# Performance work log

Measured on AMD Instinct MI355X. Metric: run time of the kernel, lower is better.

The kernel has to match this reference:

```python
import jax, jax.numpy as jnp
import numpy as np

B, T, IN, H, OUT, SIM = 256, 128, 128, 1024, 256, 4
EPS_BN = 1e-5
EPS_COS = 1e-8
NEG_SLOPE = 0.2


def setup_inputs() -> dict:
    key = jax.random.key(0)
    ks = jax.random.split(key, 12)
    rn = lambda k, s: jax.random.normal(k, s, dtype=jnp.float32) * 0.05
    return {
        "x": jax.random.normal(ks[0], (B, T, IN), dtype=jnp.float32),
        "W_emb": rn(ks[1], (H, IN)),
        "b_emb": jnp.zeros((H,), jnp.float32),
        "gamma": jnp.ones((H,), jnp.float32),
        "beta": jnp.zeros((H,), jnp.float32),
        "memory": jax.random.normal(ks[2], (1, T, H), dtype=jnp.float32),
        "w_ih_x": rn(ks[3], (3 * OUT, H)),
        "w_hh_x": rn(ks[4], (3 * OUT, OUT)),
        "b_ih_x": jnp.zeros((3 * OUT,), jnp.float32),
        "b_hh_x": jnp.zeros((3 * OUT,), jnp.float32),
        "w_ih_m": rn(ks[5], (3 * OUT, H)),
        "w_hh_m": rn(ks[6], (3 * OUT, OUT)),
        "b_ih_m": jnp.zeros((3 * OUT,), jnp.float32),
        "b_hh_m": jnp.zeros((3 * OUT,), jnp.float32),
        "W_sx": rn(ks[7], (SIM, OUT)),
        "b_sx": jnp.zeros((SIM,), jnp.float32),
        "W_sm": rn(ks[8], (SIM, OUT)),
        "b_sm": jnp.zeros((SIM,), jnp.float32),
    }


def _gru(x, h, w_ih, w_hh, b_ih, b_hh):
    # PyTorch GRUCell math
    gi = x @ w_ih.T + b_ih
    gh = h @ w_hh.T + b_hh
    i_r, i_z, i_n = jnp.split(gi, 3, axis=-1)
    h_r, h_z, h_n = jnp.split(gh, 3, axis=-1)
    r = jax.nn.sigmoid(i_r + h_r)
    z = jax.nn.sigmoid(i_z + h_z)
    n = jnp.tanh(i_n + r * h_n)
    return (1.0 - z) * n + z * h


def _forward(x, W_emb, b_emb, gamma, beta, memory,
             w_ih_x, w_hh_x, b_ih_x, b_hh_x,
             w_ih_m, w_hh_m, b_ih_m, b_hh_m,
             W_sx, b_sx, W_sm, b_sm):
    # embed + LeakyReLU(0.2)
    e = x @ W_emb.T + b_emb                                  # (B,T,H)
    e = jnp.where(e >= 0, e, NEG_SLOPE * e)
    # BatchNorm1d, training mode: per-channel stats over (B,T), biased var
    mean = jnp.mean(e, axis=(0, 1))
    var = jnp.mean((e - mean) ** 2, axis=(0, 1))
    e = (e - mean) * jax.lax.rsqrt(var + EPS_BN) * gamma + beta

    mem = memory[0]                                          # (T,H) shared across batch
    b = x.shape[0]

    def step(carry, inps):
        hx, hm = carry
        xt, mt = inps                                        # (B,H), (H,)
        mtb = jnp.broadcast_to(mt, (b, mt.shape[-1]))
        hx = _gru(xt, hx, w_ih_x, w_hh_x, b_ih_x, b_hh_x)    # (B,OUT)
        hm = _gru(mtb, hm, w_ih_m, w_hh_m, b_ih_m, b_hh_m)   # (B,OUT)
        # cosine-similarity addressing between sim_size projections
        qx = hx @ W_sx.T + b_sx                              # (B,SIM)
        qm = hm @ W_sm.T + b_sm
        num = jnp.sum(qx * qm, axis=-1)
        den = (jnp.maximum(jnp.linalg.norm(qx, axis=-1), EPS_COS)
               * jnp.maximum(jnp.linalg.norm(qm, axis=-1), EPS_COS))
        g = jax.nn.sigmoid(num / den)[:, None]               # gate in (0,1)
        out = g * hx + (1.0 - g) * hm
        return (hx, hm), out

    h0 = (jnp.zeros((b, OUT), e.dtype), jnp.zeros((b, OUT), e.dtype))
    (_, _), outs = jax.lax.scan(step, h0, (e.transpose(1, 0, 2), mem))
    return outs[-1].reshape(-1, OUT)                         # out of last timestep


def reference(x, W_emb, b_emb, gamma, beta, memory,
              w_ih_x, w_hh_x, b_ih_x, b_hh_x,
              w_ih_m, w_hh_m, b_ih_m, b_hh_m,
              W_sx, b_sx, W_sm, b_sm):
    return _forward(x, W_emb, b_emb, gamma, beta, memory,
                    w_ih_x, w_hh_x, b_ih_x, b_hh_x,
                    w_ih_m, w_hh_m, b_ih_m, b_hh_m,
                    W_sx, b_sx, W_sm, b_sm)
```

## Files before the change

kernel.cpp:

```cpp
#include <hip/hip_runtime.h>
#include <stdint.h>


typedef float  f32x4 __attribute__((ext_vector_type(4)));
typedef __bf16 bf16x8 __attribute__((ext_vector_type(8)));

#define B_   256
#define T_   128
#define IN_  128
#define H_   1024
#define OUT_ 256
#define M_   32768

static constexpr size_t OFF_XB    = 0;
static constexpr size_t OFF_WEMB  = 8388608;
static constexpr size_t OFF_WHX   = 8650752;
static constexpr size_t OFF_WHM   = 9043968;
static constexpr size_t OFF_SUM   = 9437184;
static constexpr size_t OFF_SSQ   = 9441280;
static constexpr size_t OFF_SCALE = 9445376;
static constexpr size_t OFF_CC    = 9449472;
static constexpr size_t OFF_BIASX = 9453568;
static constexpr size_t OFF_GIM   = 9457664;
static constexpr size_t OFF_EACT  = 9654272;
static constexpr size_t OFF_GI    = 76763136;
static constexpr size_t OFF_HXF   = 127094784;
static constexpr size_t OFF_HMF   = 127356928;
static constexpr size_t OFF_WPX   = 127373312;

__device__ __forceinline__ float sigmoidf_(float x) {
    return __builtin_amdgcn_rcpf(1.0f + __expf(-x));
}
__device__ __forceinline__ float tanhf_(float x) {
    return 1.0f - 2.0f * __builtin_amdgcn_rcpf(1.0f + __expf(2.0f * x));
}
__device__ __forceinline__ void gload_lds16(const void* g, void* l) {
    __builtin_amdgcn_global_load_lds(
        (const __attribute__((address_space(1))) unsigned int*)g,
        (__attribute__((address_space(3))) unsigned int*)l, 16, 0, 0);
}

__global__ void prep(const float* __restrict__ x, const float* __restrict__ wemb,
                     const float* __restrict__ whx, const float* __restrict__ whm,
                     __bf16* __restrict__ xb, __bf16* __restrict__ wembb,
                     __bf16* __restrict__ whxb, __bf16* __restrict__ whmb,
                     float* __restrict__ stats )
{
    long i = (long)blockIdx.x * 256 + threadIdx.x;
    if (i < 2048) stats[i] = 0.0f;
    if (i < 4194304)      xb[i] = (__bf16)x[i];
    else if (i < 4325376) wembb[i - 4194304] = (__bf16)wemb[i - 4194304];
    else if (i < 4521984) whxb[i - 4325376]  = (__bf16)whx[i - 4325376];
    else if (i < 4718592) whmb[i - 4521984]  = (__bf16)whm[i - 4521984];
}

template<int MODE>
__launch_bounds__(256)
__global__ void gemm_nt(const __bf16* __restrict__ A, const __bf16* __restrict__ Bm,
                        const float* __restrict__ bias, __bf16* __restrict__ C,
                        float* __restrict__ sums, float* __restrict__ ssqs,
                        int K, int N)
{
    __shared__ __bf16 As[128 * 32];
    __shared__ __bf16 Bs[128 * 32];
    const int tid  = threadIdx.x;
    const int lane = tid & 63;
    const int wv   = tid >> 6;
    const int wm   = wv >> 1, wn = wv & 1;
    const int l15  = lane & 15, quad = lane >> 4;
    const long m0 = (long)blockIdx.x * 128;
    const long n0 = (long)blockIdx.y * 128;

    const int srow = lane >> 2;
    const int scol = (lane & 3) * 8;
    const __bf16* ag[2]; const __bf16* bg[2];
    __bf16* al[2]; __bf16* bl[2];
#pragma unroll
    for (int j = 0; j < 2; j++) {
        const int s = wv * 2 + j;
        ag[j] = A  + (m0 + s * 16 + srow) * K + scol;
        bg[j] = Bm + (n0 + s * 16 + srow) * K + scol;
        al[j] = &As[s * 512];
        bl[j] = &Bs[s * 512];
    }

    const f32x4 fz = {0.f, 0.f, 0.f, 0.f};
    f32x4 acc[4][4];
#pragma unroll
    for (int i = 0; i < 4; i++)
#pragma unroll
        for (int j = 0; j < 4; j++) acc[i][j] = fz;

    for (int k0 = 0; k0 < K; k0 += 32) {
        __syncthreads();
        gload_lds16(ag[0] + k0, al[0]);
        gload_lds16(ag[1] + k0, al[1]);
        gload_lds16(bg[0] + k0, bl[0]);
        gload_lds16(bg[1] + k0, bl[1]);
        __syncthreads();
        bf16x8 af[4], bfr[4];
#pragma unroll
        for (int mt = 0; mt < 4; mt++)
            af[mt] = *(const bf16x8*)(&As[(wm * 64 + mt * 16 + l15) * 32 + quad * 8]);
#pragma unroll
        for (int nt = 0; nt < 4; nt++)
            bfr[nt] = *(const bf16x8*)(&Bs[(wn * 64 + nt * 16 + l15) * 32 + quad * 8]);
#pragma unroll
        for (int mt = 0; mt < 4; mt++)
#pragma unroll
            for (int nt = 0; nt < 4; nt++)
                acc[mt][nt] = __builtin_amdgcn_mfma_f32_16x16x32_bf16(af[mt], bfr[nt], acc[mt][nt], 0, 0, 0);
    }

#pragma unroll
    for (int nt = 0; nt < 4; nt++) {
        const long ncol = n0 + wn * 64 + nt * 16 + l15;
        const float bi = bias[ncol];
        float s = 0.f, ss = 0.f;
#pragma unroll
        for (int mt = 0; mt < 4; mt++) {
#pragma unroll
            for (int r = 0; r < 4; r++) {
                float v = acc[mt][nt][r] + bi;
                if (MODE == 0) v = (v >= 0.f) ? v : 0.2f * v;
                __bf16 hv = (__bf16)v;
                C[(m0 + wm * 64 + mt * 16 + quad * 4 + r) * (long)N + ncol] = hv;
                if (MODE == 0) { float fv = (float)hv; s += fv; ss += fv * fv; }
            }
        }
        if (MODE == 0) {
            s += __shfl_xor(s, 16);  ss += __shfl_xor(ss, 16);
            s += __shfl_xor(s, 32);  ss += __shfl_xor(ss, 32);
            if (lane < 16) {
                atomicAdd(&sums[n0 + wn * 64 + nt * 16 + lane], s);
                atomicAdd(&ssqs[n0 + wn * 64 + nt * 16 + lane], ss);
            }
        }
    }
}

__global__ void finalize_stats(const float* __restrict__ sums, const float* __restrict__ ssqs,
                               const float* __restrict__ gamma, const float* __restrict__ beta,
                               float* __restrict__ scale, float* __restrict__ cc)
{
    int h = threadIdx.x;
    const float inv = 1.0f / 32768.0f;
    float mean = sums[h] * inv;
    float var  = ssqs[h] * inv - mean * mean;
    float s    = rsqrtf(var + 1e-5f) * gamma[h];
    scale[h] = s;
    cc[h]    = beta[h] - mean * s;
}

__global__ void build_wp(const float* __restrict__ w_ih_x, const float* __restrict__ b_ih_x,
                         const float* __restrict__ b_hh_x, const float* __restrict__ scale,
                         const float* __restrict__ cc, __bf16* __restrict__ wpx,
                         float* __restrict__ biasx)
{
    const int j = blockIdx.x;
    const int lane = threadIdx.x;
    float accv = 0.f;
#pragma unroll
    for (int i = 0; i < 16; i++) {
        int h = i * 64 + lane;
        float w = w_ih_x[(long)j * 1024 + h];
        wpx[(long)j * 1024 + h] = (__bf16)(w * scale[h]);
        accv += cc[h] * w;
    }
    for (int off = 32; off; off >>= 1) accv += __shfl_xor(accv, off);
    if (lane == 0) biasx[j] = accv + b_ih_x[j] + (j < 512 ? b_hh_x[j] : 0.0f);
}

__global__ void build_gim(const float* __restrict__ memory, const float* __restrict__ w_ih_m,
                          const float* __restrict__ b_ih_m, const float* __restrict__ b_hh_m,
                          __bf16* __restrict__ gim)
{
    const int j = blockIdx.x;
    const int t0 = blockIdx.y * 32;
    const int lane = threadIdx.x;
    float w[16];
#pragma unroll
    for (int i = 0; i < 16; i++) w[i] = w_ih_m[(long)j * 1024 + i * 64 + lane];
    const float bb = b_ih_m[j] + (j < 512 ? b_hh_m[j] : 0.0f);
    for (int t = t0; t < t0 + 32; t++) {
        float s = 0.f;
#pragma unroll
        for (int i = 0; i < 16; i++) s += w[i] * memory[(long)t * 1024 + i * 64 + lane];
        for (int off = 32; off; off >>= 1) s += __shfl_xor(s, off);
        if (lane == 0) gim[t * 768 + j] = (__bf16)(s + bb);
    }
}

__launch_bounds__(512, 2)
__global__ void recurrence(const __bf16* __restrict__ gi, const __bf16* __restrict__ gim,
                           const __bf16* __restrict__ whx, const __bf16* __restrict__ whm,
                           const float* __restrict__ bhhx, const float* __restrict__ bhhm,
                           float* __restrict__ hxfin, float* __restrict__ hmfin)
{
    __shared__ __bf16 hxl[2][16 * 264];
    __shared__ __bf16 gil[2][16 * 776];
    const int wg   = blockIdx.x;
    const int tid  = threadIdx.x;
    const int lane = tid & 63;
    const int v    = tid >> 6;
    const int l15  = lane & 15, quad = lane >> 4;
    const bool isX = (wg < 16);
    const __bf16* wh    = isX ? whx : whm;
    const float*  bhh   = isX ? bhhx : bhhm;
    const __bf16* gbase = isX ? gi : gim;

    bf16x8 W[6][8];
#pragma unroll
    for (int nt = 0; nt < 6; nt++) {
        const int g = nt >> 1, ct = nt & 1;
        const long j = g * 256 + (v * 2 + ct) * 16 + l15;
#pragma unroll
        for (int kt = 0; kt < 8; kt++)
            W[nt][kt] = *(const bf16x8*)(wh + j * 256 + kt * 32 + quad * 8);
    }
    float bhhn[2];
#pragma unroll
    for (int ct = 0; ct < 2; ct++) bhhn[ct] = bhh[512 + v * 32 + ct * 16 + l15];

    for (int i = tid; i < 16 * 264; i += 512) hxl[0][i] = (__bf16)0.f;

    float st[8];
#pragma unroll
    for (int i = 0; i < 8; i++) st[i] = 0.f;

    const int r0 = v * 2, r1 = r0 + 1;
    const long grow0 = isX ? (long)((wg * 16 + r0) * 128) * 768 : 0;
    const long grow1 = isX ? (long)((wg * 16 + r1) * 128) * 768 : 0;

    {
        const __bf16* p0 = gbase + grow0;
        const __bf16* p1 = gbase + grow1;
        gload_lds16(p0 + (long)lane * 8, &gil[0][r0 * 776]);
        gload_lds16(p1 + (long)lane * 8, &gil[0][r1 * 776]);
        if (lane < 32) {
            gload_lds16(p0 + 512 + (long)lane * 8, &gil[0][r0 * 776 + 512]);
            gload_lds16(p1 + 512 + (long)lane * 8, &gil[0][r1 * 776 + 512]);
        }
    }
    __syncthreads();

    int cur = 0;
    for (int t = 0; t < 128; t++) {
        if (t < 127) {
            const __bf16* p0 = gbase + grow0 + (long)(t + 1) * 768;
            const __bf16* p1 = gbase + grow1 + (long)(t + 1) * 768;
            __bf16* dst = &gil[(t + 1) & 1][0];
            gload_lds16(p0 + (long)lane * 8, dst + r0 * 776);
            gload_lds16(p1 + (long)lane * 8, dst + r1 * 776);
            if (lane < 32) {
                gload_lds16(p0 + 512 + (long)lane * 8, dst + r0 * 776 + 512);
                gload_lds16(p1 + 512 + (long)lane * 8, dst + r1 * 776 + 512);
            }
        }

        const f32x4 fz = {0.f, 0.f, 0.f, 0.f};
        f32x4 acc[6];
#pragma unroll
        for (int nt = 0; nt < 6; nt++) acc[nt] = fz;
        const __bf16* hxc = &hxl[cur][0];
#pragma unroll
        for (int kt = 0; kt < 8; kt++) {
            bf16x8 a = *(const bf16x8*)(hxc + l15 * 264 + kt * 32 + quad * 8);
#pragma unroll
            for (int nt = 0; nt < 6; nt++)
                acc[nt] = __builtin_amdgcn_mfma_f32_16x16x32_bf16(a, W[nt][kt], acc[nt], 0, 0, 0);
        }

        const int nxt = cur ^ 1;
        __bf16* hxn = &hxl[nxt][0];
        const __bf16* gcur = &gil[t & 1][0];
#pragma unroll
        for (int ct = 0; ct < 2; ct++) {
            const int ob = v * 32 + ct * 16 + l15;
#pragma unroll
            for (int r = 0; r < 4; r++) {
                const int row = quad * 4 + r;
                const float gr = (float)gcur[row * 776 + ob];
                const float gz = (float)gcur[row * 776 + 256 + ob];
                const float gn = (float)gcur[row * 776 + 512 + ob];
                const float rg = sigmoidf_(gr + acc[ct][r]);
                const float zg = sigmoidf_(gz + acc[2 + ct][r]);
                const float ng = tanhf_(gn + rg * (acc[4 + ct][r] + bhhn[ct]));
                float h = st[ct * 4 + r];
                h = ng + zg * (h - ng);
                st[ct * 4 + r] = h;
                hxn[row * 264 + ob] = (__bf16)h;
            }
        }
        __syncthreads();
        cur = nxt;
    }

    float* finp = isX ? (hxfin + (long)wg * 16 * 256) : hmfin;
#pragma unroll
    for (int ct = 0; ct < 2; ct++) {
        const int ob = v * 32 + ct * 16 + l15;
#pragma unroll
        for (int r = 0; r < 4; r++)
            finp[(quad * 4 + r) * 256 + ob] = st[ct * 4 + r];
    }
}

__global__ void finalize(const float* __restrict__ hxfin, const float* __restrict__ hmfin,
                         const float* __restrict__ W_sx, const float* __restrict__ b_sx,
                         const float* __restrict__ W_sm, const float* __restrict__ b_sm,
                         float* __restrict__ out)
{
    const int b = blockIdx.x;
    const int lane = threadIdx.x;
    float qx[4], qm[4];
#pragma unroll
    for (int s = 0; s < 4; s++) {
        float px = 0.f, pm = 0.f;
#pragma unroll
        for (int i = 0; i < 4; i++) {
            int h = i * 64 + lane;
            px += W_sx[s * 256 + h] * hxfin[b * 256 + h];
            pm += W_sm[s * 256 + h] * hmfin[h];
        }
        for (int off = 32; off; off >>= 1) { px += __shfl_xor(px, off); pm += __shfl_xor(pm, off); }
        qx[s] = px + b_sx[s];
        qm[s] = pm + b_sm[s];
    }
    float num = 0.f, nx = 0.f, nm = 0.f;
#pragma unroll
    for (int s = 0; s < 4; s++) { num += qx[s] * qm[s]; nx += qx[s] * qx[s]; nm += qm[s] * qm[s]; }
    const float den = fmaxf(sqrtf(nx), 1e-8f) * fmaxf(sqrtf(nm), 1e-8f);
    const float g = 1.0f / (1.0f + __expf(-num / den));
#pragma unroll
    for (int i = 0; i < 4; i++) {
        int h = i * 64 + lane;
        out[b * 256 + h] = g * hxfin[b * 256 + h] + (1.0f - g) * hmfin[h];
    }
}

extern "C" void kernel_launch(void* const* d_in, const int* in_sizes, int n_in,
                              void* d_out, int out_size, void* d_ws, size_t ws_size,
                              hipStream_t stream)
{
    (void)in_sizes; (void)n_in; (void)out_size; (void)ws_size;
    const float* x      = (const float*)d_in[0];
    const float* W_emb  = (const float*)d_in[1];
    const float* b_emb  = (const float*)d_in[2];
    const float* gamma  = (const float*)d_in[3];
    const float* beta   = (const float*)d_in[4];
    const float* memory = (const float*)d_in[5];
    const float* w_ih_x = (const float*)d_in[6];
    const float* w_hh_x = (const float*)d_in[7];
    const float* b_ih_x = (const float*)d_in[8];
    const float* b_hh_x = (const float*)d_in[9];
    const float* w_ih_m = (const float*)d_in[10];
    const float* w_hh_m = (const float*)d_in[11];
    const float* b_ih_m = (const float*)d_in[12];
    const float* b_hh_m = (const float*)d_in[13];
    const float* W_sx   = (const float*)d_in[14];
    const float* b_sx   = (const float*)d_in[15];
    const float* W_sm   = (const float*)d_in[16];
    const float* b_sm   = (const float*)d_in[17];
    float* out = (float*)d_out;
    char* ws = (char*)d_ws;

    __bf16* xb    = (__bf16*)(ws + OFF_XB);
    __bf16* wembb = (__bf16*)(ws + OFF_WEMB);
    __bf16* whxb  = (__bf16*)(ws + OFF_WHX);
    __bf16* whmb  = (__bf16*)(ws + OFF_WHM);
    float*  sums  = (float*)(ws + OFF_SUM);
    float*  ssqs  = (float*)(ws + OFF_SSQ);
    float*  scale = (float*)(ws + OFF_SCALE);
    float*  cc    = (float*)(ws + OFF_CC);
    float*  biasx = (float*)(ws + OFF_BIASX);
    __bf16* gim   = (__bf16*)(ws + OFF_GIM);
    __bf16* eact  = (__bf16*)(ws + OFF_EACT);
    __bf16* gi    = (__bf16*)(ws + OFF_GI);
    float*  hxf   = (float*)(ws + OFF_HXF);
    float*  hmf   = (float*)(ws + OFF_HMF);
    __bf16* wpx   = (__bf16*)(ws + OFF_WPX);

    prep<<<18432, 256, 0, stream>>>(x, W_emb, w_hh_x, w_hh_m, xb, wembb, whxb, whmb, sums);
    gemm_nt<0><<<dim3(256, 8), 256, 0, stream>>>(xb, wembb, b_emb, eact, sums, ssqs, 128, 1024);
    finalize_stats<<<1, 1024, 0, stream>>>(sums, ssqs, gamma, beta, scale, cc);
    build_wp<<<768, 64, 0, stream>>>(w_ih_x, b_ih_x, b_hh_x, scale, cc, wpx, biasx);
    build_gim<<<dim3(768, 4), 64, 0, stream>>>(memory, w_ih_m, b_ih_m, b_hh_m, gim);
    gemm_nt<1><<<dim3(256, 6), 256, 0, stream>>>(eact, wpx, biasx, gi, sums, ssqs, 1024, 768);
    recurrence<<<17, 512, 0, stream>>>(gi, gim, whxb, whmb, b_hh_x, b_hh_m, hxf, hmf);
    finalize<<<256, 64, 0, stream>>>(hxf, hmf, W_sx, b_sx, W_sm, b_sm, out);
}
```

Measured before the change: 492.4 us.

## Split recurrence over 16 waves per block and fold BN stats into build_wp

The recurrence kernel now runs 1024 threads (16 waves) per block, each wave owning 16 output columns and one batch row's gate prefetch, instead of 8 waves each owning 32 columns. This halves the per-wave MFMA chain and register-held weights on the sequential critical path, and doubles latency hiding per step. The cost is heavier __syncthreads across more waves. Separately, the finalize_stats launch is removed, and each build_wp block recomputes mean and scale inline, trading redundant work for one fewer kernel launch.

```diff
diff --git a/kernel.cpp b/kernel.cpp
--- a/kernel.cpp
+++ b/kernel.cpp
@@ -139,33 +139,26 @@
     }
 }
 
-__global__ void finalize_stats(const float* __restrict__ sums, const float* __restrict__ ssqs,
-                               const float* __restrict__ gamma, const float* __restrict__ beta,
-                               float* __restrict__ scale, float* __restrict__ cc)
-{
-    int h = threadIdx.x;
-    const float inv = 1.0f / 32768.0f;
-    float mean = sums[h] * inv;
-    float var  = ssqs[h] * inv - mean * mean;
-    float s    = rsqrtf(var + 1e-5f) * gamma[h];
-    scale[h] = s;
-    cc[h]    = beta[h] - mean * s;
-}
-
 __global__ void build_wp(const float* __restrict__ w_ih_x, const float* __restrict__ b_ih_x,
-                         const float* __restrict__ b_hh_x, const float* __restrict__ scale,
-                         const float* __restrict__ cc, __bf16* __restrict__ wpx,
+                         const float* __restrict__ b_hh_x, const float* __restrict__ sums,
+                         const float* __restrict__ ssqs, const float* __restrict__ gamma,
+                         const float* __restrict__ beta, __bf16* __restrict__ wpx,
                          float* __restrict__ biasx)
 {
     const int j = blockIdx.x;
     const int lane = threadIdx.x;
+    const float inv = 1.0f / 32768.0f;
     float accv = 0.f;
 #pragma unroll
     for (int i = 0; i < 16; i++) {
         int h = i * 64 + lane;
+        float mean = sums[h] * inv;
+        float var  = ssqs[h] * inv - mean * mean;
+        float s    = rsqrtf(var + 1e-5f) * gamma[h];
+        float c    = beta[h] - mean * s;
         float w = w_ih_x[(long)j * 1024 + h];
-        wpx[(long)j * 1024 + h] = (__bf16)(w * scale[h]);
-        accv += cc[h] * w;
+        wpx[(long)j * 1024 + h] = (__bf16)(w * s);
+        accv += c * w;
     }
     for (int off = 32; off; off >>= 1) accv += __shfl_xor(accv, off);
     if (lane == 0) biasx[j] = accv + b_ih_x[j] + (j < 512 ? b_hh_x[j] : 0.0f);
@@ -191,7 +184,7 @@
     }
 }
 
-__launch_bounds__(512, 2)
+__launch_bounds__(1024, 4)
 __global__ void recurrence(const __bf16* __restrict__ gi, const __bf16* __restrict__ gim,
                            const __bf16* __restrict__ whx, const __bf16* __restrict__ whm,
                            const float* __restrict__ bhhx, const float* __restrict__ bhhm,
@@ -209,88 +202,72 @@
     const float*  bhh   = isX ? bhhx : bhhm;
     const __bf16* gbase = isX ? gi : gim;
 
-    bf16x8 W[6][8];
-#pragma unroll
-    for (int nt = 0; nt < 6; nt++) {
-        const int g = nt >> 1, ct = nt & 1;
-        const long j = g * 256 + (v * 2 + ct) * 16 + l15;
+    bf16x8 W[3][8];
+#pragma unroll
+    for (int g = 0; g < 3; g++) {
+        const long j = g * 256 + v * 16 + l15;
 #pragma unroll
         for (int kt = 0; kt < 8; kt++)
-            W[nt][kt] = *(const bf16x8*)(wh + j * 256 + kt * 32 + quad * 8);
-    }
-    float bhhn[2];
-#pragma unroll
-    for (int ct = 0; ct < 2; ct++) bhhn[ct] = bhh[512 + v * 32 + ct * 16 + l15];
-
-    for (int i = tid; i < 16 * 264; i += 512) hxl[0][i] = (__bf16)0.f;
-
-    float st[8];
-#pragma unroll
-    for (int i = 0; i < 8; i++) st[i] = 0.f;
-
-    const int r0 = v * 2, r1 = r0 + 1;
-    const long grow0 = isX ? (long)((wg * 16 + r0) * 128) * 768 : 0;
-    const long grow1 = isX ? (long)((wg * 16 + r1) * 128) * 768 : 0;
+            W[g][kt] = *(const bf16x8*)(wh + j * 256 + kt * 32 + quad * 8);
+    }
+    const int ob = v * 16 + l15;
+    const float bhhn = bhh[512 + ob];
+
+    for (int i = tid; i < 16 * 264; i += 1024) hxl[0][i] = (__bf16)0.f;
+
+    float st[4];
+#pragma unroll
+    for (int i = 0; i < 4; i++) st[i] = 0.f;
+
+    const long grow = isX ? (long)((wg * 16 + v) * 128) * 768 : 0;
 
     {
-        const __bf16* p0 = gbase + grow0;
-        const __bf16* p1 = gbase + grow1;
-        gload_lds16(p0 + (long)lane * 8, &gil[0][r0 * 776]);
-        gload_lds16(p1 + (long)lane * 8, &gil[0][r1 * 776]);
-        if (lane < 32) {
-            gload_lds16(p0 + 512 + (long)lane * 8, &gil[0][r0 * 776 + 512]);
-            gload_lds16(p1 + 512 + (long)lane * 8, &gil[0][r1 * 776 + 512]);
-        }
+        const __bf16* p = gbase + grow;
+        gload_lds16(p + (long)lane * 8, &gil[0][v * 776]);
+        if (lane < 32)
+            gload_lds16(p + 512 + (long)lane * 8, &gil[0][v * 776 + 512]);
     }
     __syncthreads();
 
     int cur = 0;
     for (int t = 0; t < 128; t++) {
         if (t < 127) {
-            const __bf16* p0 = gbase + grow0 + (long)(t + 1) * 768;
-            const __bf16* p1 = gbase + grow1 + (long)(t + 1) * 768;
-            __bf16* dst = &gil[(t + 1) & 1][0];
-            gload_lds16(p0 + (long)lane * 8, dst + r0 * 776);
-            gload_lds16(p1 + (long)lane * 8, dst + r1 * 776);
-            if (lane < 32) {
-                gload_lds16(p0 + 512 + (long)lane * 8, dst + r0 * 776 + 512);
-                gload_lds16(p1 + 512 + (long)lane * 8, dst + r1 * 776 + 512);
-            }
+            const __bf16* p = gbase + grow + (long)(t + 1) * 768;
+            __bf16* dst = &gil[(t + 1) & 1][v * 776];
+            gload_lds16(p + (long)lane * 8, dst);
+            if (lane < 32)
+                gload_lds16(p + 512 + (long)lane * 8, dst + 512);
         }
 
         const f32x4 fz = {0.f, 0.f, 0.f, 0.f};
-        f32x4 acc[6];
-#pragma unroll
-        for (int nt = 0; nt < 6; nt++) acc[nt] = fz;
+        f32x4 acc[3];
+#pragma unroll
+        for (int g = 0; g < 3; g++) acc[g] = fz;
         const __bf16* hxc = &hxl[cur][0];
 #pragma unroll
         for (int kt = 0; kt < 8; kt++) {
             bf16x8 a = *(const bf16x8*)(hxc + l15 * 264 + kt * 32 + quad * 8);
 #pragma unroll
-            for (int nt = 0; nt < 6; nt++)
-                acc[nt] = __builtin_amdgcn_mfma_f32_16x16x32_bf16(a, W[nt][kt], acc[nt], 0, 0, 0);
+            for (int g = 0; g < 3; g++)
+                acc[g] = __builtin_amdgcn_mfma_f32_16x16x32_bf16(a, W[g][kt], acc[g], 0, 0, 0);
         }
 
         const int nxt = cur ^ 1;
         __bf16* hxn = &hxl[nxt][0];
         const __bf16* gcur = &gil[t & 1][0];
 #pragma unroll
-        for (int ct = 0; ct < 2; ct++) {
-            const int ob = v * 32 + ct * 16 + l15;
-#pragma unroll
-            for (int r = 0; r < 4; r++) {
-                const int row = quad * 4 + r;
-                const float gr = (float)gcur[row * 776 + ob];
-                const float gz = (float)gcur[row * 776 + 256 + ob];
-                const float gn = (float)gcur[row * 776 + 512 + ob];
-                const float rg = sigmoidf_(gr + acc[ct][r]);
-                const float zg = sigmoidf_(gz + acc[2 + ct][r]);
-                const float ng = tanhf_(gn + rg * (acc[4 + ct][r] + bhhn[ct]));
-                float h = st[ct * 4 + r];
-                h = ng + zg * (h - ng);
-                st[ct * 4 + r] = h;
-                hxn[row * 264 + ob] = (__bf16)h;
-            }
+        for (int r = 0; r < 4; r++) {
+            const int row = quad * 4 + r;
+            const float gr = (float)gcur[row * 776 + ob];
+            const float gz = (float)gcur[row * 776 + 256 + ob];
+            const float gn = (float)gcur[row * 776 + 512 + ob];
+            const float rg = sigmoidf_(gr + acc[0][r]);
+            const float zg = sigmoidf_(gz + acc[1][r]);
+            const float ng = tanhf_(gn + rg * (acc[2][r] + bhhn));
+            float h = st[r];
+            h = ng + zg * (h - ng);
+            st[r] = h;
+            hxn[row * 264 + ob] = (__bf16)h;
         }
         __syncthreads();
         cur = nxt;
@@ -298,12 +275,8 @@
 
     float* finp = isX ? (hxfin + (long)wg * 16 * 256) : hmfin;
 #pragma unroll
-    for (int ct = 0; ct < 2; ct++) {
-        const int ob = v * 32 + ct * 16 + l15;
-#pragma unroll
-        for (int r = 0; r < 4; r++)
-            finp[(quad * 4 + r) * 256 + ob] = st[ct * 4 + r];
-    }
+    for (int r = 0; r < 4; r++)
+        finp[(quad * 4 + r) * 256 + ob] = st[r];
 }
 
 __global__ void finalize(const float* __restrict__ hxfin, const float* __restrict__ hmfin,
@@ -371,8 +344,6 @@
     __bf16* whmb  = (__bf16*)(ws + OFF_WHM);
     float*  sums  = (float*)(ws + OFF_SUM);
     float*  ssqs  = (float*)(ws + OFF_SSQ);
-    float*  scale = (float*)(ws + OFF_SCALE);
-    float*  cc    = (float*)(ws + OFF_CC);
     float*  biasx = (float*)(ws + OFF_BIASX);
     __bf16* gim   = (__bf16*)(ws + OFF_GIM);
     __bf16* eact  = (__bf16*)(ws + OFF_EACT);
@@ -383,10 +354,9 @@
 
     prep<<<18432, 256, 0, stream>>>(x, W_emb, w_hh_x, w_hh_m, xb, wembb, whxb, whmb, sums);
     gemm_nt<0><<<dim3(256, 8), 256, 0, stream>>>(xb, wembb, b_emb, eact, sums, ssqs, 128, 1024);
-    finalize_stats<<<1, 1024, 0, stream>>>(sums, ssqs, gamma, beta, scale, cc);
-    build_wp<<<768, 64, 0, stream>>>(w_ih_x, b_ih_x, b_hh_x, scale, cc, wpx, biasx);
+    build_wp<<<768, 64, 0, stream>>>(w_ih_x, b_ih_x, b_hh_x, sums, ssqs, gamma, beta, wpx, biasx);
     build_gim<<<dim3(768, 4), 64, 0, stream>>>(memory, w_ih_m, b_ih_m, b_hh_m, gim);
     gemm_nt<1><<<dim3(256, 6), 256, 0, stream>>>(eact, wpx, biasx, gi, sums, ssqs, 1024, 768);
-    recurrence<<<17, 512, 0, stream>>>(gi, gim, whxb, whmb, b_hh_x, b_hh_m, hxf, hmf);
+    recurrence<<<17, 1024, 0, stream>>>(gi, gim, whxb, whmb, b_hh_x, b_hh_m, hxf, hmf);
     finalize<<<256, 64, 0, stream>>>(hxf, hmf, W_sx, b_sx, W_sm, b_sm, out);
 }
```

Measured after the change: 538.7 us. 9.4% more time.

## Overlap input-projection GEMM with recurrence via flag-synchronized fused kernel

Applied to the files above, without the earlier changes.

Merges the gi GEMM and the recurrence into one launch. Blocks 17 and up compute 128-row tiles of gi in time-major order and publish per-tile completion flags. The 17 recurrence blocks spin on those flags, so the sequential recurrence can start while later timesteps are still being projected. The BN stats finalization is folded into the weight-prep kernel, which now also builds gim, cutting several launches. The cost is spin-waiting, GEMM tiles shrinking to 128x128 with no double buffering, and reliance on the recurrence blocks being scheduled first and on forward progress.

```diff
diff --git a/kernel.cpp b/kernel.cpp
--- a/kernel.cpp
+++ b/kernel.cpp
@@ -18,8 +18,7 @@
 static constexpr size_t OFF_WHM   = 9043968;
 static constexpr size_t OFF_SUM   = 9437184;
 static constexpr size_t OFF_SSQ   = 9441280;
-static constexpr size_t OFF_SCALE = 9445376;
-static constexpr size_t OFF_CC    = 9449472;
+static constexpr size_t OFF_FLAGS = 9445376;
 static constexpr size_t OFF_BIASX = 9453568;
 static constexpr size_t OFF_GIM   = 9457664;
 static constexpr size_t OFF_EACT  = 9654272;
@@ -44,22 +43,22 @@
                      const float* __restrict__ whx, const float* __restrict__ whm,
                      __bf16* __restrict__ xb, __bf16* __restrict__ wembb,
                      __bf16* __restrict__ whxb, __bf16* __restrict__ whmb,
-                     float* __restrict__ stats )
+                     float* __restrict__ stats , int* __restrict__ flags )
 {
     long i = (long)blockIdx.x * 256 + threadIdx.x;
     if (i < 2048) stats[i] = 0.0f;
+    else if (i < 2304) flags[i - 2048] = 0;
     if (i < 4194304)      xb[i] = (__bf16)x[i];
     else if (i < 4325376) wembb[i - 4194304] = (__bf16)wemb[i - 4194304];
     else if (i < 4521984) whxb[i - 4325376]  = (__bf16)whx[i - 4325376];
     else if (i < 4718592) whmb[i - 4521984]  = (__bf16)whm[i - 4521984];
 }
 
-template<int MODE>
 __launch_bounds__(256)
-__global__ void gemm_nt(const __bf16* __restrict__ A, const __bf16* __restrict__ Bm,
-                        const float* __restrict__ bias, __bf16* __restrict__ C,
-                        float* __restrict__ sums, float* __restrict__ ssqs,
-                        int K, int N)
+__global__ void gemm_e(const __bf16* __restrict__ A, const __bf16* __restrict__ Bm,
+                       const float* __restrict__ bias, __bf16* __restrict__ C,
+                       float* __restrict__ sums, float* __restrict__ ssqs,
+                       int K, int N)
 {
     __shared__ __bf16 As[128 * 32];
     __shared__ __bf16 Bs[128 * 32];
@@ -122,88 +121,147 @@
 #pragma unroll
             for (int r = 0; r < 4; r++) {
                 float v = acc[mt][nt][r] + bi;
-                if (MODE == 0) v = (v >= 0.f) ? v : 0.2f * v;
+                v = (v >= 0.f) ? v : 0.2f * v;
                 __bf16 hv = (__bf16)v;
                 C[(m0 + wm * 64 + mt * 16 + quad * 4 + r) * (long)N + ncol] = hv;
-                if (MODE == 0) { float fv = (float)hv; s += fv; ss += fv * fv; }
+                float fv = (float)hv; s += fv; ss += fv * fv;
             }
         }
-        if (MODE == 0) {
-            s += __shfl_xor(s, 16);  ss += __shfl_xor(ss, 16);
-            s += __shfl_xor(s, 32);  ss += __shfl_xor(ss, 32);
-            if (lane < 16) {
-                atomicAdd(&sums[n0 + wn * 64 + nt * 16 + lane], s);
-                atomicAdd(&ssqs[n0 + wn * 64 + nt * 16 + lane], ss);
-            }
-        }
-    }
-}
-
-__global__ void finalize_stats(const float* __restrict__ sums, const float* __restrict__ ssqs,
-                               const float* __restrict__ gamma, const float* __restrict__ beta,
-                               float* __restrict__ scale, float* __restrict__ cc)
-{
-    int h = threadIdx.x;
-    const float inv = 1.0f / 32768.0f;
-    float mean = sums[h] * inv;
-    float var  = ssqs[h] * inv - mean * mean;
-    float s    = rsqrtf(var + 1e-5f) * gamma[h];
-    scale[h] = s;
-    cc[h]    = beta[h] - mean * s;
-}
-
-__global__ void build_wp(const float* __restrict__ w_ih_x, const float* __restrict__ b_ih_x,
-                         const float* __restrict__ b_hh_x, const float* __restrict__ scale,
-                         const float* __restrict__ cc, __bf16* __restrict__ wpx,
-                         float* __restrict__ biasx)
-{
-    const int j = blockIdx.x;
+        s += __shfl_xor(s, 16);  ss += __shfl_xor(ss, 16);
+        s += __shfl_xor(s, 32);  ss += __shfl_xor(ss, 32);
+        if (lane < 16) {
+            atomicAdd(&sums[n0 + wn * 64 + nt * 16 + lane], s);
+            atomicAdd(&ssqs[n0 + wn * 64 + nt * 16 + lane], ss);
+        }
+    }
+}
+
+__global__ void build_misc(const float* __restrict__ w_ih_x, const float* __restrict__ b_ih_x,
+                           const float* __restrict__ b_hh_x, const float* __restrict__ sums,
+                           const float* __restrict__ ssqs, const float* __restrict__ gamma,
+                           const float* __restrict__ beta, __bf16* __restrict__ wpx,
+                           float* __restrict__ biasx,
+                           const float* __restrict__ memory, const float* __restrict__ w_ih_m,
+                           const float* __restrict__ b_ih_m, const float* __restrict__ b_hh_m,
+                           __bf16* __restrict__ gim)
+{
     const int lane = threadIdx.x;
-    float accv = 0.f;
-#pragma unroll
-    for (int i = 0; i < 16; i++) {
-        int h = i * 64 + lane;
-        float w = w_ih_x[(long)j * 1024 + h];
-        wpx[(long)j * 1024 + h] = (__bf16)(w * scale[h]);
-        accv += cc[h] * w;
-    }
-    for (int off = 32; off; off >>= 1) accv += __shfl_xor(accv, off);
-    if (lane == 0) biasx[j] = accv + b_ih_x[j] + (j < 512 ? b_hh_x[j] : 0.0f);
-}
-
-__global__ void build_gim(const float* __restrict__ memory, const float* __restrict__ w_ih_m,
-                          const float* __restrict__ b_ih_m, const float* __restrict__ b_hh_m,
-                          __bf16* __restrict__ gim)
-{
-    const int j = blockIdx.x;
-    const int t0 = blockIdx.y * 32;
-    const int lane = threadIdx.x;
-    float w[16];
-#pragma unroll
-    for (int i = 0; i < 16; i++) w[i] = w_ih_m[(long)j * 1024 + i * 64 + lane];
-    const float bb = b_ih_m[j] + (j < 512 ? b_hh_m[j] : 0.0f);
-    for (int t = t0; t < t0 + 32; t++) {
-        float s = 0.f;
-#pragma unroll
-        for (int i = 0; i < 16; i++) s += w[i] * memory[(long)t * 1024 + i * 64 + lane];
-        for (int off = 32; off; off >>= 1) s += __shfl_xor(s, off);
-        if (lane == 0) gim[t * 768 + j] = (__bf16)(s + bb);
+    if (blockIdx.x < 768) {
+        const int j = blockIdx.x;
+        const float inv = 1.0f / 32768.0f;
+        float accv = 0.f;
+#pragma unroll
+        for (int i = 0; i < 16; i++) {
+            int h = i * 64 + lane;
+            float mean = sums[h] * inv;
+            float var  = ssqs[h] * inv - mean * mean;
+            float s    = rsqrtf(var + 1e-5f) * gamma[h];
+            float c    = beta[h] - mean * s;
+            float w = w_ih_x[(long)j * 1024 + h];
+            wpx[(long)j * 1024 + h] = (__bf16)(w * s);
+            accv += c * w;
+        }
+        for (int off = 32; off; off >>= 1) accv += __shfl_xor(accv, off);
+        if (lane == 0) biasx[j] = accv + b_ih_x[j] + (j < 512 ? b_hh_x[j] : 0.0f);
+    } else {
+        const int g = blockIdx.x - 768;
+        const int j = g & 1023 % 1024;
+        const int jj = g % 768;
+        const int t0 = (g / 768) * 32;
+        float w[16];
+#pragma unroll
+        for (int i = 0; i < 16; i++) w[i] = w_ih_m[(long)jj * 1024 + i * 64 + lane];
+        const float bb = b_ih_m[jj] + (jj < 512 ? b_hh_m[jj] : 0.0f);
+        for (int t = t0; t < t0 + 32; t++) {
+            float s = 0.f;
+#pragma unroll
+            for (int i = 0; i < 16; i++) s += w[i] * memory[(long)t * 1024 + i * 64 + lane];
+            for (int off = 32; off; off >>= 1) s += __shfl_xor(s, off);
+            if (lane == 0) gim[t * 768 + jj] = (__bf16)(s + bb);
+        }
+        (void)j;
     }
 }
 
 __launch_bounds__(512, 2)
-__global__ void recurrence(const __bf16* __restrict__ gi, const __bf16* __restrict__ gim,
-                           const __bf16* __restrict__ whx, const __bf16* __restrict__ whm,
-                           const float* __restrict__ bhhx, const float* __restrict__ bhhm,
-                           float* __restrict__ hxfin, float* __restrict__ hmfin)
-{
-    __shared__ __bf16 hxl[2][16 * 264];
-    __shared__ __bf16 gil[2][16 * 776];
-    const int wg   = blockIdx.x;
+__global__ void fused(const __bf16* __restrict__ eact, const __bf16* __restrict__ wpx,
+                      const float* __restrict__ biasx, __bf16* __restrict__ gi,
+                      const __bf16* __restrict__ gim,
+                      const __bf16* __restrict__ whx, const __bf16* __restrict__ whm,
+                      const float* __restrict__ bhhx, const float* __restrict__ bhhm,
+                      float* __restrict__ hxfin, float* __restrict__ hmfin,
+                      int* __restrict__ flags)
+{
+    __shared__ union {
+        struct { __bf16 hxl[2][16 * 264]; __bf16 gil[2][16 * 776]; } rec;
+        struct { __bf16 As[128 * 32]; __bf16 Bs[128 * 32]; } gm;
+        char pad[83968];
+    } sm;
+
     const int tid  = threadIdx.x;
     const int lane = tid & 63;
     const int v    = tid >> 6;
     const int l15  = lane & 15, quad = lane >> 4;
+
+    if (blockIdx.x >= 17) {
+        const int g  = blockIdx.x - 17;
+        const int mt = g / 6;
+        const long m0 = (long)mt * 128;
+        const long n0 = (long)(g % 6) * 128;
+        const int wm = v >> 1, wn = v & 1;
+
+        const int srow = lane >> 2;
+        const int scol = (lane & 3) * 8;
+        const long m = m0 + v * 16 + srow;
+        const __bf16* agA = eact + (((m & 255) << 7) + (m >> 8)) * 1024 + scol;
+        const __bf16* agB = wpx + (n0 + v * 16 + srow) * 1024 + scol;
+        __bf16* alA = &sm.gm.As[v * 512];
+        __bf16* alB = &sm.gm.Bs[v * 512];
+
+        const f32x4 fz = {0.f, 0.f, 0.f, 0.f};
+        f32x4 acc[2][4];
+#pragma unroll
+        for (int i = 0; i < 2; i++)
+#pragma unroll
+            for (int j = 0; j < 4; j++) acc[i][j] = fz;
+
+        for (int k0 = 0; k0 < 1024; k0 += 32) {
+            __syncthreads();
+            gload_lds16(agA + k0, alA);
+            gload_lds16(agB + k0, alB);
+            __syncthreads();
+            bf16x8 af[2], bfr[4];
+#pragma unroll
+            for (int i = 0; i < 2; i++)
+                af[i] = *(const bf16x8*)(&sm.gm.As[(wm * 32 + i * 16 + l15) * 32 + quad * 8]);
+#pragma unroll
+            for (int j = 0; j < 4; j++)
+                bfr[j] = *(const bf16x8*)(&sm.gm.Bs[(wn * 64 + j * 16 + l15) * 32 + quad * 8]);
+#pragma unroll
+            for (int i = 0; i < 2; i++)
+#pragma unroll
+                for (int j = 0; j < 4; j++)
+                    acc[i][j] = __builtin_amdgcn_mfma_f32_16x16x32_bf16(af[i], bfr[j], acc[i][j], 0, 0, 0);
+        }
+
+#pragma unroll
+        for (int j = 0; j < 4; j++) {
+            const long ncol = n0 + wn * 64 + j * 16 + l15;
+            const float bi = biasx[ncol];
+#pragma unroll
+            for (int i = 0; i < 2; i++)
+#pragma unroll
+                for (int r = 0; r < 4; r++)
+                    gi[(m0 + wm * 32 + i * 16 + quad * 4 + r) * 768 + ncol] =
+                        (__bf16)(acc[i][j][r] + bi);
+        }
+        __syncthreads();
+        if (tid == 0)
+            __hip_atomic_fetch_add(&flags[mt], 1, __ATOMIC_RELEASE, __HIP_MEMORY_SCOPE_AGENT);
+        return;
+    }
+
+    const int wg   = blockIdx.x;
     const bool isX = (wg < 16);
     const __bf16* wh    = isX ? whx : whm;
     const float*  bhh   = isX ? bhhx : bhhm;
@@ -212,8 +270,8 @@
     bf16x8 W[6][8];
 #pragma unroll
     for (int nt = 0; nt < 6; nt++) {
-        const int g = nt >> 1, ct = nt & 1;
-        const long j = g * 256 + (v * 2 + ct) * 16 + l15;
+        const int gg = nt >> 1, ct = nt & 1;
+        const long j = gg * 256 + (v * 2 + ct) * 16 + l15;
 #pragma unroll
         for (int kt = 0; kt < 8; kt++)
             W[nt][kt] = *(const bf16x8*)(wh + j * 256 + kt * 32 + quad * 8);
@@ -222,24 +280,36 @@
 #pragma unroll
     for (int ct = 0; ct < 2; ct++) bhhn[ct] = bhh[512 + v * 32 + ct * 16 + l15];
 
-    for (int i = tid; i < 16 * 264; i += 512) hxl[0][i] = (__bf16)0.f;
+    for (int i = tid; i < 16 * 264; i += 512) sm.rec.hxl[0][i] = (__bf16)0.f;
 
     float st[8];
 #pragma unroll
     for (int i = 0; i < 8; i++) st[i] = 0.f;
 
     const int r0 = v * 2, r1 = r0 + 1;
-    const long grow0 = isX ? (long)((wg * 16 + r0) * 128) * 768 : 0;
-    const long grow1 = isX ? (long)((wg * 16 + r1) * 128) * 768 : 0;
-
+    const long base0 = isX ? (long)(wg * 16 + r0) * 768 : 0;
+    const long base1 = isX ? (long)(wg * 16 + r1) * 768 : 0;
+    const long tstr  = isX ? (long)256 * 768 : 768;
+    const int  myhalf = wg >> 3;
+
+    int ready = -1;
+    if (isX) {
+        const int need = myhalf;
+        if (__hip_atomic_load(&flags[need], __ATOMIC_ACQUIRE, __HIP_MEMORY_SCOPE_AGENT) == 6) ready = need;
+        else {
+            while (__hip_atomic_load(&flags[need], __ATOMIC_ACQUIRE, __HIP_MEMORY_SCOPE_AGENT) != 6)
+                __builtin_amdgcn_s_sleep(2);
+            ready = need;
+        }
+    }
     {
-        const __bf16* p0 = gbase + grow0;
-        const __bf16* p1 = gbase + grow1;
-        gload_lds16(p0 + (long)lane * 8, &gil[0][r0 * 776]);
-        gload_lds16(p1 + (long)lane * 8, &gil[0][r1 * 776]);
+        const __bf16* p0 = gbase + base0;
+        const __bf16* p1 = gbase + base1;
+        gload_lds16(p0 + (long)lane * 8, &sm.rec.gil[0][r0 * 776]);
+        gload_lds16(p1 + (long)lane * 8, &sm.rec.gil[0][r1 * 776]);
         if (lane < 32) {
-            gload_lds16(p0 + 512 + (long)lane * 8, &gil[0][r0 * 776 + 512]);
-            gload_lds16(p1 + 512 + (long)lane * 8, &gil[0][r1 * 776 + 512]);
+            gload_lds16(p0 + 512 + (long)lane * 8, &sm.rec.gil[0][r0 * 776 + 512]);
+            gload_lds16(p1 + 512 + (long)lane * 8, &sm.rec.gil[0][r1 * 776 + 512]);
         }
     }
     __syncthreads();
@@ -247,9 +317,22 @@
     int cur = 0;
     for (int t = 0; t < 128; t++) {
         if (t < 127) {
-            const __bf16* p0 = gbase + grow0 + (long)(t + 1) * 768;
-            const __bf16* p1 = gbase + grow1 + (long)(t + 1) * 768;
-            __bf16* dst = &gil[(t + 1) & 1][0];
+            if (isX) {
+                const int need = 2 * (t + 1) + myhalf;
+                if (need > ready) {
+                    int probe = need + 14; if (probe > 255) probe = 255;
+                    if (__hip_atomic_load(&flags[probe], __ATOMIC_ACQUIRE, __HIP_MEMORY_SCOPE_AGENT) == 6)
+                        ready = probe;
+                    else {
+                        while (__hip_atomic_load(&flags[need], __ATOMIC_ACQUIRE, __HIP_MEMORY_SCOPE_AGENT) != 6)
+                            __builtin_amdgcn_s_sleep(2);
+                        ready = need;
+                    }
+                }
+            }
+            const __bf16* p0 = gbase + base0 + (long)(t + 1) * tstr;
+            const __bf16* p1 = gbase + base1 + (long)(t + 1) * tstr;
+            __bf16* dst = &sm.rec.gil[(t + 1) & 1][0];
             gload_lds16(p0 + (long)lane * 8, dst + r0 * 776);
             gload_lds16(p1 + (long)lane * 8, dst + r1 * 776);
             if (lane < 32) {
@@ -262,7 +345,7 @@
         f32x4 acc[6];
 #pragma unroll
         for (int nt = 0; nt < 6; nt++) acc[nt] = fz;
-        const __bf16* hxc = &hxl[cur][0];
+        const __bf16* hxc = &sm.rec.hxl[cur][0];
 #pragma unroll
         for (int kt = 0; kt < 8; kt++) {
             bf16x8 a = *(const bf16x8*)(hxc + l15 * 264 + kt * 32 + quad * 8);
@@ -272,8 +355,8 @@
         }
 
         const int nxt = cur ^ 1;
-        __bf16* hxn = &hxl[nxt][0];
-        const __bf16* gcur = &gil[t & 1][0];
+        __bf16* hxn = &sm.rec.hxl[nxt][0];
+        const __bf16* gcur = &sm.rec.gil[t & 1][0];
 #pragma unroll
         for (int ct = 0; ct < 2; ct++) {
             const int ob = v * 32 + ct * 16 + l15;
@@ -371,8 +454,7 @@
     __bf16* whmb  = (__bf16*)(ws + OFF_WHM);
     float*  sums  = (float*)(ws + OFF_SUM);
     float*  ssqs  = (float*)(ws + OFF_SSQ);
-    float*  scale = (float*)(ws + OFF_SCALE);
-    float*  cc    = (float*)(ws + OFF_CC);
+    int*    flags = (int*)(ws + OFF_FLAGS);
     float*  biasx = (float*)(ws + OFF_BIASX);
     __bf16* gim   = (__bf16*)(ws + OFF_GIM);
     __bf16* eact  = (__bf16*)(ws + OFF_EACT);
@@ -381,12 +463,11 @@
     float*  hmf   = (float*)(ws + OFF_HMF);
     __bf16* wpx   = (__bf16*)(ws + OFF_WPX);
 
-    prep<<<18432, 256, 0, stream>>>(x, W_emb, w_hh_x, w_hh_m, xb, wembb, whxb, whmb, sums);
-    gemm_nt<0><<<dim3(256, 8), 256, 0, stream>>>(xb, wembb, b_emb, eact, sums, ssqs, 128, 1024);
-    finalize_stats<<<1, 1024, 0, stream>>>(sums, ssqs, gamma, beta, scale, cc);
-    build_wp<<<768, 64, 0, stream>>>(w_ih_x, b_ih_x, b_hh_x, scale, cc, wpx, biasx);
-    build_gim<<<dim3(768, 4), 64, 0, stream>>>(memory, w_ih_m, b_ih_m, b_hh_m, gim);
-    gemm_nt<1><<<dim3(256, 6), 256, 0, stream>>>(eact, wpx, biasx, gi, sums, ssqs, 1024, 768);
-    recurrence<<<17, 512, 0, stream>>>(gi, gim, whxb, whmb, b_hh_x, b_hh_m, hxf, hmf);
+    prep<<<18432, 256, 0, stream>>>(x, W_emb, w_hh_x, w_hh_m, xb, wembb, whxb, whmb, sums, flags);
+    gemm_e<<<dim3(256, 8), 256, 0, stream>>>(xb, wembb, b_emb, eact, sums, ssqs, 128, 1024);
+    build_misc<<<3840, 64, 0, stream>>>(w_ih_x, b_ih_x, b_hh_x, sums, ssqs, gamma, beta, wpx, biasx,
+                                        memory, w_ih_m, b_ih_m, b_hh_m, gim);
+    fused<<<17 + 1536, 512, 0, stream>>>(eact, wpx, biasx, gi, gim, whxb, whmb,
+                                         b_hh_x, b_hh_m, hxf, hmf, flags);
     finalize<<<256, 64, 0, stream>>>(hxf, hmf, W_sx, b_sx, W_sm, b_sm, out);
 }
```

Measured after the change: 490.2 us. About the same (-0.4%).

## Merge stats/weight-prep kernels and retile input-gate GEMM to 256x384 blocks

Applied to the files above, without the earlier changes.

Folds finalize_stats, build_wp and build_gim into one build_misc launch, recomputing the BN scale and shift inline per channel so the scale/cc buffers go away. The gi GEMM (K=1024, N=768) now uses a dedicated 1024-thread kernel with 256x384 tiles instead of the generic 128x128 template. Bigger tiles raise operand reuse and cut global reloads of A and B, and fewer launches cut launch overhead. The cost is 256 blocks, roughly one per CU, with more accumulators per thread, which may lower latency hiding. The k-loop is still unpipelined.

```diff
diff --git a/kernel.cpp b/kernel.cpp
--- a/kernel.cpp
+++ b/kernel.cpp
@@ -4,13 +4,6 @@
 
 typedef float  f32x4 __attribute__((ext_vector_type(4)));
 typedef __bf16 bf16x8 __attribute__((ext_vector_type(8)));
-
-#define B_   256
-#define T_   128
-#define IN_  128
-#define H_   1024
-#define OUT_ 256
-#define M_   32768
 
 static constexpr size_t OFF_XB    = 0;
 static constexpr size_t OFF_WEMB  = 8388608;
@@ -18,8 +11,6 @@
 static constexpr size_t OFF_WHM   = 9043968;
 static constexpr size_t OFF_SUM   = 9437184;
 static constexpr size_t OFF_SSQ   = 9441280;
-static constexpr size_t OFF_SCALE = 9445376;
-static constexpr size_t OFF_CC    = 9449472;
 static constexpr size_t OFF_BIASX = 9453568;
 static constexpr size_t OFF_GIM   = 9457664;
 static constexpr size_t OFF_EACT  = 9654272;
@@ -54,12 +45,11 @@
     else if (i < 4718592) whmb[i - 4521984]  = (__bf16)whm[i - 4521984];
 }
 
-template<int MODE>
 __launch_bounds__(256)
-__global__ void gemm_nt(const __bf16* __restrict__ A, const __bf16* __restrict__ Bm,
-                        const float* __restrict__ bias, __bf16* __restrict__ C,
-                        float* __restrict__ sums, float* __restrict__ ssqs,
-                        int K, int N)
+__global__ void gemm_e(const __bf16* __restrict__ A, const __bf16* __restrict__ Bm,
+                       const float* __restrict__ bias, __bf16* __restrict__ C,
+                       float* __restrict__ sums, float* __restrict__ ssqs,
+                       int K, int N)
 {
     __shared__ __bf16 As[128 * 32];
     __shared__ __bf16 Bs[128 * 32];
@@ -122,72 +112,126 @@
 #pragma unroll
             for (int r = 0; r < 4; r++) {
                 float v = acc[mt][nt][r] + bi;
-                if (MODE == 0) v = (v >= 0.f) ? v : 0.2f * v;
+                v = (v >= 0.f) ? v : 0.2f * v;
                 __bf16 hv = (__bf16)v;
                 C[(m0 + wm * 64 + mt * 16 + quad * 4 + r) * (long)N + ncol] = hv;
-                if (MODE == 0) { float fv = (float)hv; s += fv; ss += fv * fv; }
+                float fv = (float)hv; s += fv; ss += fv * fv;
             }
         }
-        if (MODE == 0) {
-            s += __shfl_xor(s, 16);  ss += __shfl_xor(ss, 16);
-            s += __shfl_xor(s, 32);  ss += __shfl_xor(ss, 32);
-            if (lane < 16) {
-                atomicAdd(&sums[n0 + wn * 64 + nt * 16 + lane], s);
-                atomicAdd(&ssqs[n0 + wn * 64 + nt * 16 + lane], ss);
-            }
-        }
-    }
-}
-
-__global__ void finalize_stats(const float* __restrict__ sums, const float* __restrict__ ssqs,
-                               const float* __restrict__ gamma, const float* __restrict__ beta,
-                               float* __restrict__ scale, float* __restrict__ cc)
-{
-    int h = threadIdx.x;
-    const float inv = 1.0f / 32768.0f;
-    float mean = sums[h] * inv;
-    float var  = ssqs[h] * inv - mean * mean;
-    float s    = rsqrtf(var + 1e-5f) * gamma[h];
-    scale[h] = s;
-    cc[h]    = beta[h] - mean * s;
-}
-
-__global__ void build_wp(const float* __restrict__ w_ih_x, const float* __restrict__ b_ih_x,
-                         const float* __restrict__ b_hh_x, const float* __restrict__ scale,
-                         const float* __restrict__ cc, __bf16* __restrict__ wpx,
-                         float* __restrict__ biasx)
-{
-    const int j = blockIdx.x;
+        s += __shfl_xor(s, 16);  ss += __shfl_xor(ss, 16);
+        s += __shfl_xor(s, 32);  ss += __shfl_xor(ss, 32);
+        if (lane < 16) {
+            atomicAdd(&sums[n0 + wn * 64 + nt * 16 + lane], s);
+            atomicAdd(&ssqs[n0 + wn * 64 + nt * 16 + lane], ss);
+        }
+    }
+}
+
+__global__ void build_misc(const float* __restrict__ w_ih_x, const float* __restrict__ b_ih_x,
+                           const float* __restrict__ b_hh_x, const float* __restrict__ sums,
+                           const float* __restrict__ ssqs, const float* __restrict__ gamma,
+                           const float* __restrict__ beta, __bf16* __restrict__ wpx,
+                           float* __restrict__ biasx,
+                           const float* __restrict__ memory, const float* __restrict__ w_ih_m,
+                           const float* __restrict__ b_ih_m, const float* __restrict__ b_hh_m,
+                           __bf16* __restrict__ gim)
+{
     const int lane = threadIdx.x;
-    float accv = 0.f;
-#pragma unroll
-    for (int i = 0; i < 16; i++) {
-        int h = i * 64 + lane;
-        float w = w_ih_x[(long)j * 1024 + h];
-        wpx[(long)j * 1024 + h] = (__bf16)(w * scale[h]);
-        accv += cc[h] * w;
-    }
-    for (int off = 32; off; off >>= 1) accv += __shfl_xor(accv, off);
-    if (lane == 0) biasx[j] = accv + b_ih_x[j] + (j < 512 ? b_hh_x[j] : 0.0f);
-}
-
-__global__ void build_gim(const float* __restrict__ memory, const float* __restrict__ w_ih_m,
-                          const float* __restrict__ b_ih_m, const float* __restrict__ b_hh_m,
-                          __bf16* __restrict__ gim)
-{
-    const int j = blockIdx.x;
-    const int t0 = blockIdx.y * 32;
-    const int lane = threadIdx.x;
-    float w[16];
-#pragma unroll
-    for (int i = 0; i < 16; i++) w[i] = w_ih_m[(long)j * 1024 + i * 64 + lane];
-    const float bb = b_ih_m[j] + (j < 512 ? b_hh_m[j] : 0.0f);
-    for (int t = t0; t < t0 + 32; t++) {
-        float s = 0.f;
-#pragma unroll
-        for (int i = 0; i < 16; i++) s += w[i] * memory[(long)t * 1024 + i * 64 + lane];
-        for (int off = 32; off; off >>= 1) s += __shfl_xor(s, off);
-        if (lane == 0) gim[t * 768 + j] = (__bf16)(s + bb);
+    if (blockIdx.x < 768) {
+        const int j = blockIdx.x;
+        const float inv = 1.0f / 32768.0f;
+        float accv = 0.f;
+#pragma unroll
+        for (int i = 0; i < 16; i++) {
+            int h = i * 64 + lane;
+            float mean = sums[h] * inv;
+            float var  = ssqs[h] * inv - mean * mean;
+            float s    = rsqrtf(var + 1e-5f) * gamma[h];
+            float c    = beta[h] - mean * s;
+            float w = w_ih_x[(long)j * 1024 + h];
+            wpx[(long)j * 1024 + h] = (__bf16)(w * s);
+            accv += c * w;
+        }
+        for (int off = 32; off; off >>= 1) accv += __shfl_xor(accv, off);
+        if (lane == 0) biasx[j] = accv + b_ih_x[j] + (j < 512 ? b_hh_x[j] : 0.0f);
+    } else {
+        const int g  = blockIdx.x - 768;
+        const int jj = g % 768;
+        const int t0 = (g / 768) * 32;
+        float w[16];
+#pragma unroll
+        for (int i = 0; i < 16; i++) w[i] = w_ih_m[(long)jj * 1024 + i * 64 + lane];
+        const float bb = b_ih_m[jj] + (jj < 512 ? b_hh_m[jj] : 0.0f);
+        for (int t = t0; t < t0 + 32; t++) {
+            float s = 0.f;
+#pragma unroll
+            for (int i = 0; i < 16; i++) s += w[i] * memory[(long)t * 1024 + i * 64 + lane];
+            for (int off = 32; off; off >>= 1) s += __shfl_xor(s, off);
+            if (lane == 0) gim[t * 768 + jj] = (__bf16)(s + bb);
+        }
+    }
+}
+
+__launch_bounds__(1024)
+__global__ void gemm_gi3(const __bf16* __restrict__ A, const __bf16* __restrict__ Bm,
+                         const float* __restrict__ bias, __bf16* __restrict__ C)
+{
+    __shared__ __bf16 As[256 * 32];
+    __shared__ __bf16 Bs[384 * 32];
+    const int tid  = threadIdx.x;
+    const int lane = tid & 63;
+    const int v    = tid >> 6;
+    const int l15  = lane & 15, quad = lane >> 4;
+    const int wm   = v >> 2, wn = v & 3;
+    const long m0 = (long)blockIdx.x * 256;
+    const long n0 = (long)blockIdx.y * 384;
+
+    const int srow = lane >> 2;
+    const int scol = (lane & 3) * 8;
+    const __bf16* ag  = A  + (m0 + v * 16 + srow) * 1024 + scol;
+    __bf16*       al  = &As[v * 512];
+    const __bf16* bg0 = Bm + (n0 + v * 16 + srow) * 1024 + scol;
+    __bf16*       bl0 = &Bs[v * 512];
+    const __bf16* bg1 = Bm + (n0 + 256 + v * 16 + srow) * 1024 + scol;
+    __bf16*       bl1 = &Bs[(16 + v) * 512];
+
+    const f32x4 fz = {0.f, 0.f, 0.f, 0.f};
+    f32x4 acc[4][6];
+#pragma unroll
+    for (int i = 0; i < 4; i++)
+#pragma unroll
+        for (int j = 0; j < 6; j++) acc[i][j] = fz;
+
+    for (int k0 = 0; k0 < 1024; k0 += 32) {
+        __syncthreads();
+        gload_lds16(ag + k0, al);
+        gload_lds16(bg0 + k0, bl0);
+        if (v < 8) gload_lds16(bg1 + k0, bl1);
+        __syncthreads();
+        bf16x8 af[4], bfr[6];
+#pragma unroll
+        for (int i = 0; i < 4; i++)
+            af[i] = *(const bf16x8*)(&As[(wm * 64 + i * 16 + l15) * 32 + quad * 8]);
+#pragma unroll
+        for (int j = 0; j < 6; j++)
+            bfr[j] = *(const bf16x8*)(&Bs[(wn * 96 + j * 16 + l15) * 32 + quad * 8]);
+#pragma unroll
+        for (int i = 0; i < 4; i++)
+#pragma unroll
+            for (int j = 0; j < 6; j++)
+                acc[i][j] = __builtin_amdgcn_mfma_f32_16x16x32_bf16(af[i], bfr[j], acc[i][j], 0, 0, 0);
+    }
+
+#pragma unroll
+    for (int j = 0; j < 6; j++) {
+        const long ncol = n0 + wn * 96 + j * 16 + l15;
+        const float bi = bias[ncol];
+#pragma unroll
+        for (int i = 0; i < 4; i++)
+#pragma unroll
+            for (int r = 0; r < 4; r++)
+                C[(m0 + wm * 64 + i * 16 + quad * 4 + r) * 768 + ncol] =
+                    (__bf16)(acc[i][j][r] + bi);
     }
 }
 
@@ -371,8 +415,6 @@
     __bf16* whmb  = (__bf16*)(ws + OFF_WHM);
     float*  sums  = (float*)(ws + OFF_SUM);
     float*  ssqs  = (float*)(ws + OFF_SSQ);
-    float*  scale = (float*)(ws + OFF_SCALE);
-    float*  cc    = (float*)(ws + OFF_CC);
     float*  biasx = (float*)(ws + OFF_BIASX);
     __bf16* gim   = (__bf16*)(ws + OFF_GIM);
     __bf16* eact  = (__bf16*)(ws + OFF_EACT);
@@ -382,11 +424,10 @@
     __bf16* wpx   = (__bf16*)(ws + OFF_WPX);
 
     prep<<<18432, 256, 0, stream>>>(x, W_emb, w_hh_x, w_hh_m, xb, wembb, whxb, whmb, sums);
-    gemm_nt<0><<<dim3(256, 8), 256, 0, stream>>>(xb, wembb, b_emb, eact, sums, ssqs, 128, 1024);
-    finalize_stats<<<1, 1024, 0, stream>>>(sums, ssqs, gamma, beta, scale, cc);
-    build_wp<<<768, 64, 0, stream>>>(w_ih_x, b_ih_x, b_hh_x, scale, cc, wpx, biasx);
-    build_gim<<<dim3(768, 4), 64, 0, stream>>>(memory, w_ih_m, b_ih_m, b_hh_m, gim);
-    gemm_nt<1><<<dim3(256, 6), 256, 0, stream>>>(eact, wpx, biasx, gi, sums, ssqs, 1024, 768);
+    gemm_e<<<dim3(256, 8), 256, 0, stream>>>(xb, wembb, b_emb, eact, sums, ssqs, 128, 1024);
+    build_misc<<<3840, 64, 0, stream>>>(w_ih_x, b_ih_x, b_hh_x, sums, ssqs, gamma, beta, wpx, biasx,
+                                        memory, w_ih_m, b_ih_m, b_hh_m, gim);
+    gemm_gi3<<<dim3(128, 2), 1024, 0, stream>>>(eact, wpx, biasx, gi);
     recurrence<<<17, 512, 0, stream>>>(gi, gim, whxb, whmb, b_hh_x, b_hh_m, hxf, hmf);
     finalize<<<256, 64, 0, stream>>>(hxf, hmf, W_sx, b_sx, W_sm, b_sm, out);
 }
```

Measured after the change: 552.4 us. 1.12x slower.
